# Kernel optimization log

Measured on AMD Instinct MI355X. Metric: run time of the kernel, lower is better.

## Reference

```python
import jax, jax.numpy as jnp
import numpy as np

HEADS = 8
DIM_HEAD = 64


def setup_inputs() -> dict:
    key = jax.random.key(0)
    ks = jax.random.split(key, 7)
    b, c, h, w = 8, 256, 64, 64
    hidden = HEADS * DIM_HEAD  # 512
    return {
        "x": jax.random.normal(ks[0], (b, c, h, w), dtype=jnp.float32),
        "context": jax.random.normal(ks[1], (b, c, h, w), dtype=jnp.float32),
        "Wq": jax.random.normal(ks[2], (hidden, c), dtype=jnp.float32) * 0.02,
        "Wk": jax.random.normal(ks[3], (hidden, c), dtype=jnp.float32) * 0.02,
        "Wv": jax.random.normal(ks[4], (hidden, c), dtype=jnp.float32) * 0.02,
        "Wo": jax.random.normal(ks[5], (c, hidden), dtype=jnp.float32) * 0.02,
        "bo": jnp.zeros((c,), dtype=jnp.float32),
    }


def reference(x, context, Wq, Wk, Wv, Wo, bo):
    b, c, h, w = x.shape
    n = h * w
    scale = DIM_HEAD ** (-0.5)
    xf = x.reshape(b, c, n)                      # b c n
    cf = context.reshape(b, context.shape[1], -1)  # b c m
    # 1x1 convs == per-pixel linear projections
    q = jnp.einsum('bcn,oc->bon', xf, Wq).reshape(b, HEADS, DIM_HEAD, n) * scale
    k = jnp.einsum('bcm,oc->bom', cf, Wk).reshape(b, HEADS, DIM_HEAD, -1)
    v = jnp.einsum('bcm,oc->bom', cf, Wv).reshape(b, HEADS, DIM_HEAD, -1)
    k = jax.nn.softmax(k, axis=-1)               # softmax over spatial positions
    ctx = jnp.einsum('bhdm,bhem->bhde', k, v)    # small d x e context
    out = jnp.einsum('bhde,bhdn->bhen', ctx, q)  # b h e n
    out = out.reshape(b, HEADS * DIM_HEAD, h, w)
    return jnp.einsum('bchw,oc->bohw', out, Wo) + bo[None, :, None, None]
```

## Files before the change

### kernel.cpp

```cpp
#include <hip/hip_runtime.h>

#define B   8
#define C   256
#define N   4096
#define H   8
#define D   64
#define HID 512
#define SCALE 0.125f

typedef __attribute__((ext_vector_type(8))) __bf16 bf16x8;
typedef __attribute__((ext_vector_type(4))) float f32x4;

__device__ __forceinline__ ushort bfbits(float f) {
  union { __bf16 h; ushort u; } c; c.h = (__bf16)f; return c.u;
}

__device__ __forceinline__ f32x4 mfma16(bf16x8 a, bf16x8 b, f32x4 c) {
  return __builtin_amdgcn_mfma_f32_16x16x32_bf16(a, b, c, 0, 0, 0);
}

__device__ __forceinline__ void glds16(const ushort* g, ushort* l) {
  __builtin_amdgcn_global_load_lds(
      (const __attribute__((address_space(1))) void*)g,
      (__attribute__((address_space(3))) void*)l, 16, 0, 0);
}

__global__ __launch_bounds__(256) void prep_kernel(
    const float* __restrict__ x, const float* __restrict__ ctxt,
    const float* __restrict__ Wk, const float* __restrict__ Wv,
    ushort* __restrict__ x_bf, ushort* __restrict__ ctxt_bf,
    ushort* __restrict__ wk_bf, ushort* __restrict__ wv_bf,
    float* __restrict__ ctxn, float* __restrict__ z_sum) {
  const int z = blockIdx.z;
  const int tid = threadIdx.x;
  if (z == 16) {
    const int id = blockIdx.y * 64 + blockIdx.x;
    if (id < 128) {
      const int t = (id * 256 + tid) * 4;
      const float4 a = *(const float4*)(Wk + t);
      const float4 b = *(const float4*)(Wv + t);
      ushort4 ra, rb;
      ra.x = bfbits(a.x); ra.y = bfbits(a.y); ra.z = bfbits(a.z); ra.w = bfbits(a.w);
      rb.x = bfbits(b.x); rb.y = bfbits(b.y); rb.z = bfbits(b.z); rb.w = bfbits(b.w);
      *(ushort4*)(wk_bf + t) = ra;
      *(ushort4*)(wv_bf + t) = rb;
    } else {
      const int zb = id - 128;
      const float4 zz = {0.f, 0.f, 0.f, 0.f};
      *(float4*)(ctxn + (size_t)(zb * 512 + tid) * 4) = zz;
      *(float4*)(ctxn + (size_t)(zb * 512 + 256 + tid) * 4) = zz;
      if (zb < 4) *(float4*)(z_sum + (size_t)(zb * 256 + tid) * 4) = zz;
    }
    return;
  }
  __shared__ float tile[64 * 65];
  const int b = z & 7;
  const float* src = (z < 8) ? ctxt : x;
  ushort* dst = (z < 8) ? ctxt_bf : x_bf;
  const int l0 = blockIdx.x * 64, r0 = blockIdx.y * 64;
  const int rr = tid >> 4, c4 = (tid & 15) << 2;
  const float* sp = src + ((size_t)b * C + r0) * N + l0;
#pragma unroll
  for (int p = 0; p < 4; ++p) {
    const float4 v = *(const float4*)(sp + (size_t)(rr + p * 16) * N + c4);
    float* tp = tile + (rr + p * 16) * 65 + c4;
    tp[0] = v.x; tp[1] = v.y; tp[2] = v.z; tp[3] = v.w;
  }
  __syncthreads();
  const int lr = tid >> 2, rb = (tid & 3) << 4;
  uint pk[8];
#pragma unroll
  for (int k = 0; k < 16; k += 2) {
    const uint lo = bfbits(tile[(rb + k) * 65 + lr]);
    const uint hi = bfbits(tile[(rb + k + 1) * 65 + lr]);
    pk[k >> 1] = lo | (hi << 16);
  }
  ushort* dp = dst + ((size_t)b * N + l0 + lr) * C + r0 + rb;
  *(uint4*)dp = *(uint4*)pk;
  *(uint4*)(dp + 8) = *(uint4*)(pk + 4);
}

__global__ __launch_bounds__(256, 4) void kv_mfma_kernel(
    const ushort* __restrict__ ctxt_bf,
    const ushort* __restrict__ wk_bf,
    const ushort* __restrict__ wv_bf,
    float* __restrict__ ctxn,
    float* __restrict__ z_sum)
{
  __shared__ __align__(16) ushort cb_s[2][32 * 256];
  __shared__ __align__(16) ushort p_s[64 * 32];
  __shared__ __align__(16) ushort v_s[64 * 32];
  const int mt = blockIdx.x, h = blockIdx.y, b = blockIdx.z;
  const int tid = threadIdx.x;
  const int w = tid >> 6, lane = tid & 63;
  const int col = lane & 15, quad = lane >> 4;
  const int dw = w * 16;
  const int swc = (col & 3) ^ ((col >> 2) & 3);

  const ushort* wkp = wk_bf + (size_t)(h * 64 + dw + col) * C + quad * 8;
  const ushort* wvp = wv_bf + (size_t)(h * 64 + dw + col) * C + quad * 8;
  const ushort* cbase = ctxt_bf + ((size_t)b * N + (size_t)mt * 256) * C;

  bf16x8 wkf[8], wvf[8];
#pragma unroll
  for (int kk = 0; kk < 8; ++kk) {
    wkf[kk] = *(const bf16x8*)(wkp + (size_t)kk * 32);
    wvf[kk] = *(const bf16x8*)(wvp + (size_t)kk * 32);
  }

  const int grow0 = w * 8 + (lane >> 5);
  const int ggran = lane & 31;

  const f32x4 z4 = {0.f, 0.f, 0.f, 0.f};
  f32x4 cacc[4];
#pragma unroll
  for (int j = 0; j < 4; ++j) cacc[j] = z4;
  float zl = 0.f;

#pragma unroll
  for (int it = 0; it < 4; ++it) {
    const int row = grow0 + it * 2;
    glds16(cbase + (size_t)row * C + ((ggran ^ (row & 7)) << 3),
           &cb_s[0][(w * 8 + it * 2) * 256]);
  }
  __syncthreads();

  for (int t = 0; t < 8; ++t) {
    const int cur = t & 1;
    if (t < 7) {
      const ushort* nb = cbase + (size_t)(t + 1) * 32 * C;
#pragma unroll
      for (int it = 0; it < 4; ++it) {
        const int row = grow0 + it * 2;
        glds16(nb + (size_t)row * C + ((ggran ^ (row & 7)) << 3),
               &cb_s[cur ^ 1][(w * 8 + it * 2) * 256]);
      }
    }

    f32x4 kacc[2], vacc[2];
#pragma unroll
    for (int i = 0; i < 2; ++i) { kacc[i] = z4; vacc[i] = z4; }
    __builtin_amdgcn_s_setprio(1);
#pragma unroll
    for (int kk = 0; kk < 8; ++kk) {
      bf16x8 a[2];
#pragma unroll
      for (int i = 0; i < 2; ++i) {
        const int r = i * 16 + col;
        a[i] = *(const bf16x8*)(&cb_s[cur][r * 256 +
                  ((((kk << 2) + quad) ^ (r & 7)) << 3)]);
      }
#pragma unroll
      for (int i = 0; i < 2; ++i) {
        kacc[i] = mfma16(a[i], wkf[kk], kacc[i]);
        vacc[i] = mfma16(a[i], wvf[kk], vacc[i]);
      }
    }
    __builtin_amdgcn_s_setprio(0);

#pragma unroll
    for (int i = 0; i < 2; ++i) {
      const int off = (dw + col) * 32 +
                      (((i * 2 + (quad >> 1)) ^ swc) << 3) + ((quad & 1) << 2);
      const f32x4 k4 = kacc[i];
      const float e0 = __expf(k4[0]), e1 = __expf(k4[1]);
      const float e2 = __expf(k4[2]), e3 = __expf(k4[3]);
      zl += (e0 + e1) + (e2 + e3);
      ushort4 pk; pk.x = bfbits(e0); pk.y = bfbits(e1);
      pk.z = bfbits(e2); pk.w = bfbits(e3);
      *(ushort4*)(p_s + off) = pk;
      const f32x4 v4 = vacc[i];
      ushort4 vk; vk.x = bfbits(v4[0]); vk.y = bfbits(v4[1]);
      vk.z = bfbits(v4[2]); vk.w = bfbits(v4[3]);
      *(ushort4*)(v_s + off) = vk;
    }
    __syncthreads();

    {
      const int g = (quad ^ swc) << 3;
      const bf16x8 pa = *(const bf16x8*)(p_s + (dw + col) * 32 + g);
      bf16x8 vb[4];
#pragma unroll
      for (int j = 0; j < 4; ++j)
        vb[j] = *(const bf16x8*)(v_s + (j * 16 + col) * 32 + g);
      __builtin_amdgcn_s_setprio(1);
#pragma unroll
      for (int j = 0; j < 4; ++j) cacc[j] = mfma16(pa, vb[j], cacc[j]);
      __builtin_amdgcn_s_setprio(0);
    }
    __syncthreads();
  }

  {
    float s = zl;
    s += __shfl_xor(s, 16); s += __shfl_xor(s, 32);
    if (quad == 0)
      atomicAdd(&z_sum[(size_t)(b * H + h) * 64 + dw + col], s);
  }

  float* outp = ctxn + (size_t)(b * H + h) * 4096;
#pragma unroll
  for (int j = 0; j < 4; ++j)
#pragma unroll
    for (int r = 0; r < 4; ++r)
      atomicAdd(&outp[(size_t)(dw + quad * 4 + r) * 64 + j * 16 + col],
                cacc[j][r]);
}

__global__ __launch_bounds__(256) void a_kernel(
    const float* __restrict__ ctxn, const float* __restrict__ z_sum,
    const float* __restrict__ Wq, float* __restrict__ A)
{
  const int bh = blockIdx.x, cti = blockIdx.y, tid = threadIdx.x;
  const int b = bh >> 3, h = bh & 7;
  const int c0 = cti << 6;
  __shared__ float ct[64 * 65];
  __shared__ float wq[64 * 68];
  __shared__ float zs[64];
  if (tid < 64) zs[tid] = SCALE / z_sum[(size_t)bh * 64 + tid];
  for (int r = 0; r < 16; ++r) {
    const int idx = tid + (r << 8);
    ct[(idx & 63) * 65 + (idx >> 6)] = ctxn[((size_t)bh << 12) + idx];
    wq[(idx >> 6) * 68 + (idx & 63)] =
        Wq[(size_t)(h * 64 + (idx >> 6)) * C + c0 + (idx & 63)];
  }
  __syncthreads();
  const int e = tid & 63, co = tid >> 6;
  float acc[16];
#pragma unroll
  for (int k = 0; k < 16; ++k) acc[k] = 0.f;
  for (int d = 0; d < 64; ++d) {
    const float cv = ct[e * 65 + d] * zs[d];
    const float* wr = wq + d * 68 + co * 16;
#pragma unroll
    for (int k = 0; k < 16; ++k) acc[k] += cv * wr[k];
  }
  float* Ar = A + ((size_t)b * HID + h * 64 + e) * C + c0 + co * 16;
#pragma unroll
  for (int k = 0; k < 16; ++k) Ar[k] = acc[k];
}

__global__ __launch_bounds__(256) void m_kernel(
    const float* __restrict__ A, const float* __restrict__ Wo,
    ushort* __restrict__ M_bf)
{
  const int tile = blockIdx.x, b = blockIdx.y;
  const int o0 = (tile & 7) << 5, c0 = (tile >> 3) << 6;
  const int tid = threadIdx.x, tx = tid & 15, ty = tid >> 4;
  __shared__ float wo_s[64 * 33];
  __shared__ float a_s[64 * 68];
  float acc[2][4] = {{0.f}};
  const int wo_o = tid >> 3, wo_k = (tid & 7) << 3;
  const int a_k = tid >> 2, a_c = (tid & 3) << 4;
  float4 wr0, wr1, ar0, ar1, ar2, ar3;
  {
    const float* wp = Wo + (size_t)(o0 + wo_o) * HID + wo_k;
    wr0 = *(const float4*)wp; wr1 = *(const float4*)(wp + 4);
    const float* ap = A + ((size_t)b * HID + a_k) * C + c0 + a_c;
    ar0 = *(const float4*)ap;       ar1 = *(const float4*)(ap + 4);
    ar2 = *(const float4*)(ap + 8); ar3 = *(const float4*)(ap + 12);
  }
  for (int t = 0; t < 8; ++t) {
    __syncthreads();
    {
      float* wd = wo_s + wo_k * 33 + wo_o;
      wd[0]   = wr0.x; wd[33]  = wr0.y; wd[66]  = wr0.z; wd[99]  = wr0.w;
      wd[132] = wr1.x; wd[165] = wr1.y; wd[198] = wr1.z; wd[231] = wr1.w;
      float* ad = a_s + a_k * 68 + a_c;
      *(float4*)ad = ar0;       *(float4*)(ad + 4) = ar1;
      *(float4*)(ad + 8) = ar2; *(float4*)(ad + 12) = ar3;
    }
    __syncthreads();
    if (t < 7) {
      const int k0 = (t + 1) << 6;
      const float* wp = Wo + (size_t)(o0 + wo_o) * HID + k0 + wo_k;
      wr0 = *(const float4*)wp; wr1 = *(const float4*)(wp + 4);
      const float* ap = A + ((size_t)b * HID + k0 + a_k) * C + c0 + a_c;
      ar0 = *(const float4*)ap;       ar1 = *(const float4*)(ap + 4);
      ar2 = *(const float4*)(ap + 8); ar3 = *(const float4*)(ap + 12);
    }
#pragma unroll
    for (int kc = 0; kc < 64; ++kc) {
      const float2 wv = *(const float2*)(wo_s + kc * 33 + ty * 2);
      const float4 av = *(const float4*)(a_s + kc * 68 + tx * 4);
      acc[0][0] += wv.x * av.x; acc[0][1] += wv.x * av.y;
      acc[0][2] += wv.x * av.z; acc[0][3] += wv.x * av.w;
      acc[1][0] += wv.y * av.x; acc[1][1] += wv.y * av.y;
      acc[1][2] += wv.y * av.z; acc[1][3] += wv.y * av.w;
    }
  }
#pragma unroll
  for (int i = 0; i < 2; ++i) {
    ushort4 r;
    r.x = bfbits(acc[i][0]); r.y = bfbits(acc[i][1]);
    r.z = bfbits(acc[i][2]); r.w = bfbits(acc[i][3]);
    *(ushort4*)(M_bf + ((size_t)b * C + o0 + ty * 2 + i) * C + c0 + tx * 4) = r;
  }
}

__global__ __launch_bounds__(256, 4) void out_mfma_kernel(
    const ushort* __restrict__ M_bf,
    const ushort* __restrict__ x_bf,
    const float* __restrict__ bo, float* __restrict__ out)
{
  const int nt = blockIdx.x, ot = blockIdx.y, b = blockIdx.z;
  const int tid = threadIdx.x;
  const int w = tid >> 6, lane = tid & 63;
  const int col = lane & 15, quad = lane >> 4;
  const int o0 = ot * 32;
  const size_t n_base = (size_t)nt * 256 + w * 64;
  const ushort* Ab = M_bf + ((size_t)b * C + o0 + col) * C + quad * 8;
  const ushort* Bb = x_bf + ((size_t)b * N + n_base) * C + quad * 8;

  const f32x4 z4 = {0.f, 0.f, 0.f, 0.f};
  f32x4 acc[2][4];
#pragma unroll
  for (int i = 0; i < 2; ++i)
#pragma unroll
    for (int j = 0; j < 4; ++j) acc[i][j] = z4;

#pragma unroll
  for (int kk = 0; kk < 8; ++kk) {
    bf16x8 af[2], bfz[4];
#pragma unroll
    for (int i = 0; i < 2; ++i)
      af[i] = *(const bf16x8*)(Ab + (size_t)(i * 16) * C + kk * 32);
#pragma unroll
    for (int j = 0; j < 4; ++j)
      bfz[j] = *(const bf16x8*)(Bb + (size_t)(j * 16 + col) * C + kk * 32);
#pragma unroll
    for (int i = 0; i < 2; ++i)
#pragma unroll
      for (int j = 0; j < 4; ++j) acc[i][j] = mfma16(af[i], bfz[j], acc[i][j]);
  }

#pragma unroll
  for (int i = 0; i < 2; ++i)
#pragma unroll
    for (int r = 0; r < 4; ++r) {
      const int o = o0 + i * 16 + quad * 4 + r;
      const float bias = bo[o];
      float* op = out + ((size_t)b * C + o) * N + n_base + col;
#pragma unroll
      for (int j = 0; j < 4; ++j) op[j * 16] = acc[i][j][r] + bias;
    }
}

extern "C" void kernel_launch(void* const* d_in, const int* in_sizes, int n_in,
                              void* d_out, int out_size, void* d_ws, size_t ws_size,
                              hipStream_t stream) {
  const float* x    = (const float*)d_in[0];
  const float* ctxt = (const float*)d_in[1];
  const float* Wq   = (const float*)d_in[2];
  const float* Wk   = (const float*)d_in[3];
  const float* Wv   = (const float*)d_in[4];
  const float* Wo   = (const float*)d_in[5];
  const float* bo   = (const float*)d_in[6];
  float* out = (float*)d_out;

  char* p = (char*)d_ws;
  ushort* ctxt_bf = (ushort*)p;  p += (size_t)B * N * C * 2;
  ushort* x_bf    = (ushort*)p;  p += (size_t)B * N * C * 2;
  ushort* wk_bf   = (ushort*)p;  p += (size_t)HID * C * 2;
  ushort* wv_bf   = (ushort*)p;  p += (size_t)HID * C * 2;
  ushort* M_bf    = (ushort*)p;  p += (size_t)B * C * C * 2;
  float*  z_sum   = (float*)p;   p += (size_t)B * H * 64 * 4;
  float*  ctxn    = (float*)p;   p += (size_t)B * H * D * D * 4;
  float*  A       = (float*)p;   p += (size_t)B * HID * C * 4;

  prep_kernel<<<dim3(N / 64, C / 64, 17), 256, 0, stream>>>(
      x, ctxt, Wk, Wv, x_bf, ctxt_bf, wk_bf, wv_bf, ctxn, z_sum);
  kv_mfma_kernel<<<dim3(16, H, B), 256, 0, stream>>>(
      ctxt_bf, wk_bf, wv_bf, ctxn, z_sum);
  a_kernel<<<dim3(B * H, 4), 256, 0, stream>>>(ctxn, z_sum, Wq, A);
  m_kernel<<<dim3(32, B), 256, 0, stream>>>(A, Wo, M_bf);
  out_mfma_kernel<<<dim3(N / 256, C / 32, B), 256, 0, stream>>>(M_bf, x_bf, bo, out);
}
```

Baseline: 236.0 us.

## Replace atomic context accumulation with partial buffers and add XCD-aware output block mapping

Result: no change. 237.1 us (+0.5%).

```diff
diff --git a/kernel.cpp b/kernel.cpp
--- a/kernel.cpp
+++ b/kernel.cpp
@@ -29,28 +29,20 @@
     const float* __restrict__ x, const float* __restrict__ ctxt,
     const float* __restrict__ Wk, const float* __restrict__ Wv,
     ushort* __restrict__ x_bf, ushort* __restrict__ ctxt_bf,
-    ushort* __restrict__ wk_bf, ushort* __restrict__ wv_bf,
-    float* __restrict__ ctxn, float* __restrict__ z_sum) {
+    ushort* __restrict__ wk_bf, ushort* __restrict__ wv_bf) {
   const int z = blockIdx.z;
   const int tid = threadIdx.x;
   if (z == 16) {
     const int id = blockIdx.y * 64 + blockIdx.x;
-    if (id < 128) {
-      const int t = (id * 256 + tid) * 4;
-      const float4 a = *(const float4*)(Wk + t);
-      const float4 b = *(const float4*)(Wv + t);
-      ushort4 ra, rb;
-      ra.x = bfbits(a.x); ra.y = bfbits(a.y); ra.z = bfbits(a.z); ra.w = bfbits(a.w);
-      rb.x = bfbits(b.x); rb.y = bfbits(b.y); rb.z = bfbits(b.z); rb.w = bfbits(b.w);
-      *(ushort4*)(wk_bf + t) = ra;
-      *(ushort4*)(wv_bf + t) = rb;
-    } else {
-      const int zb = id - 128;
-      const float4 zz = {0.f, 0.f, 0.f, 0.f};
-      *(float4*)(ctxn + (size_t)(zb * 512 + tid) * 4) = zz;
-      *(float4*)(ctxn + (size_t)(zb * 512 + 256 + tid) * 4) = zz;
-      if (zb < 4) *(float4*)(z_sum + (size_t)(zb * 256 + tid) * 4) = zz;
-    }
+    if (id >= 128) return;
+    const int t = (id * 256 + tid) * 4;
+    const float4 a = *(const float4*)(Wk + t);
+    const float4 b = *(const float4*)(Wv + t);
+    ushort4 ra, rb;
+    ra.x = bfbits(a.x); ra.y = bfbits(a.y); ra.z = bfbits(a.z); ra.w = bfbits(a.w);
+    rb.x = bfbits(b.x); rb.y = bfbits(b.y); rb.z = bfbits(b.z); rb.w = bfbits(b.w);
+    *(ushort4*)(wk_bf + t) = ra;
+    *(ushort4*)(wv_bf + t) = rb;
     return;
   }
   __shared__ float tile[64 * 65];
@@ -84,8 +76,8 @@
     const ushort* __restrict__ ctxt_bf,
     const ushort* __restrict__ wk_bf,
     const ushort* __restrict__ wv_bf,
-    float* __restrict__ ctxn,
-    float* __restrict__ z_sum)
+    float* __restrict__ ctx_part,
+    float* __restrict__ z_part)
 {
   __shared__ __align__(16) ushort cb_s[2][32 * 256];
   __shared__ __align__(16) ushort p_s[64 * 32];
@@ -195,29 +187,47 @@
     float s = zl;
     s += __shfl_xor(s, 16); s += __shfl_xor(s, 32);
     if (quad == 0)
-      atomicAdd(&z_sum[(size_t)(b * H + h) * 64 + dw + col], s);
-  }
-
-  float* outp = ctxn + (size_t)(b * H + h) * 4096;
+      z_part[((size_t)(b * H + h) * 16 + mt) * 64 + dw + col] = s;
+  }
+
+  float* outp = ctx_part + ((size_t)(b * H + h) * 16 + mt) * 4096;
 #pragma unroll
   for (int j = 0; j < 4; ++j)
 #pragma unroll
     for (int r = 0; r < 4; ++r)
-      atomicAdd(&outp[(size_t)(dw + quad * 4 + r) * 64 + j * 16 + col],
-                cacc[j][r]);
+      outp[(size_t)(dw + quad * 4 + r) * 64 + j * 16 + col] = cacc[j][r];
+}
+
+__global__ __launch_bounds__(256) void combine_kernel(
+    const float* __restrict__ ctx_part, const float* __restrict__ z_part,
+    float* __restrict__ ctxn)
+{
+  const int bh = blockIdx.x, seg = blockIdx.y, tid = threadIdx.x;
+  __shared__ float zs[64];
+  if (tid < 64) {
+    float z = 0.f;
+#pragma unroll
+    for (int p = 0; p < 16; ++p) z += z_part[((size_t)bh * 16 + p) * 64 + tid];
+    zs[tid] = SCALE / z;
+  }
+  __syncthreads();
+  const int idx = (seg << 8) + tid;
+  const float* cp = ctx_part + (size_t)bh * 16 * 4096;
+  float s = 0.f;
+#pragma unroll
+  for (int p = 0; p < 16; ++p) s += cp[(size_t)p * 4096 + idx];
+  ctxn[((size_t)bh << 12) + idx] = s * zs[idx >> 6];
 }
 
 __global__ __launch_bounds__(256) void a_kernel(
-    const float* __restrict__ ctxn, const float* __restrict__ z_sum,
-    const float* __restrict__ Wq, float* __restrict__ A)
+    const float* __restrict__ ctxn, const float* __restrict__ Wq,
+    float* __restrict__ A)
 {
   const int bh = blockIdx.x, cti = blockIdx.y, tid = threadIdx.x;
   const int b = bh >> 3, h = bh & 7;
   const int c0 = cti << 6;
   __shared__ float ct[64 * 65];
   __shared__ float wq[64 * 68];
-  __shared__ float zs[64];
-  if (tid < 64) zs[tid] = SCALE / z_sum[(size_t)bh * 64 + tid];
   for (int r = 0; r < 16; ++r) {
     const int idx = tid + (r << 8);
     ct[(idx & 63) * 65 + (idx >> 6)] = ctxn[((size_t)bh << 12) + idx];
@@ -230,7 +240,7 @@
 #pragma unroll
   for (int k = 0; k < 16; ++k) acc[k] = 0.f;
   for (int d = 0; d < 64; ++d) {
-    const float cv = ct[e * 65 + d] * zs[d];
+    const float cv = ct[e * 65 + d];
     const float* wr = wq + d * 68 + co * 16;
 #pragma unroll
     for (int k = 0; k < 16; ++k) acc[k] += cv * wr[k];
@@ -303,7 +313,11 @@
     const ushort* __restrict__ x_bf,
     const float* __restrict__ bo, float* __restrict__ out)
 {
-  const int nt = blockIdx.x, ot = blockIdx.y, b = blockIdx.z;
+  const int r = blockIdx.x + 16 * blockIdx.y + 128 * blockIdx.z;
+  const int xcd = r & 7, slot = r >> 3;
+  const int grp = xcd * 16 + (slot >> 3);
+  const int ot = slot & 7;
+  const int b = grp >> 4, nt = grp & 15;
   const int tid = threadIdx.x;
   const int w = tid >> 6, lane = tid & 63;
   const int col = lane & 15, quad = lane >> 4;
@@ -337,12 +351,12 @@
 #pragma unroll
   for (int i = 0; i < 2; ++i)
 #pragma unroll
-    for (int r = 0; r < 4; ++r) {
-      const int o = o0 + i * 16 + quad * 4 + r;
+    for (int r2 = 0; r2 < 4; ++r2) {
+      const int o = o0 + i * 16 + quad * 4 + r2;
       const float bias = bo[o];
       float* op = out + ((size_t)b * C + o) * N + n_base + col;
 #pragma unroll
-      for (int j = 0; j < 4; ++j) op[j * 16] = acc[i][j][r] + bias;
+      for (int j = 0; j < 4; ++j) op[j * 16] = acc[i][j][r2] + bias;
     }
 }
 
@@ -364,15 +378,17 @@
   ushort* wk_bf   = (ushort*)p;  p += (size_t)HID * C * 2;
   ushort* wv_bf   = (ushort*)p;  p += (size_t)HID * C * 2;
   ushort* M_bf    = (ushort*)p;  p += (size_t)B * C * C * 2;
-  float*  z_sum   = (float*)p;   p += (size_t)B * H * 64 * 4;
+  float*  z_part  = (float*)p;   p += (size_t)B * H * 16 * 64 * 4;
   float*  ctxn    = (float*)p;   p += (size_t)B * H * D * D * 4;
-  float*  A       = (float*)p;   p += (size_t)B * HID * C * 4;
+  float*  ctx_part= (float*)p;   p += (size_t)B * H * 16 * 4096 * 4;
+  float*  A       = ctx_part;
 
   prep_kernel<<<dim3(N / 64, C / 64, 17), 256, 0, stream>>>(
-      x, ctxt, Wk, Wv, x_bf, ctxt_bf, wk_bf, wv_bf, ctxn, z_sum);
+      x, ctxt, Wk, Wv, x_bf, ctxt_bf, wk_bf, wv_bf);
   kv_mfma_kernel<<<dim3(16, H, B), 256, 0, stream>>>(
-      ctxt_bf, wk_bf, wv_bf, ctxn, z_sum);
-  a_kernel<<<dim3(B * H, 4), 256, 0, stream>>>(ctxn, z_sum, Wq, A);
+      ctxt_bf, wk_bf, wv_bf, ctx_part, z_part);
+  combine_kernel<<<dim3(B * H, 16), 256, 0, stream>>>(ctx_part, z_part, ctxn);
+  a_kernel<<<dim3(B * H, 4), 256, 0, stream>>>(ctxn, Wq, A);
   m_kernel<<<dim3(32, B), 256, 0, stream>>>(A, Wo, M_bf);
   out_mfma_kernel<<<dim3(N / 256, C / 32, B), 256, 0, stream>>>(M_bf, x_bf, bo, out);
 }
```
